# Kernel tuning notes

Hardware: AMD Instinct MI355X
Metric: run time of the kernel (lower is better)

Reference implementation:

```python
import jax, jax.numpy as jnp
import numpy as np

N_NODES = 50000


def setup_inputs() -> dict:
    key = jax.random.key(0)
    k1, k2, k3, k4, k5 = jax.random.split(key, 5)
    N, E, D_IN, D_OUT = N_NODES, 800000, 128, 128
    features = jax.random.normal(k1, (N, D_IN), dtype=jnp.float32)
    src = jax.random.randint(k2, (E,), 0, N, dtype=jnp.int32)
    dst = jax.random.randint(k3, (E,), 0, N, dtype=jnp.int32)
    # Kaiming-ish init for linear weights
    W_self = jax.random.normal(k4, (D_IN, D_OUT), dtype=jnp.float32) / np.sqrt(D_IN)
    W_neigh = jax.random.normal(k5, (D_IN, D_OUT), dtype=jnp.float32) / np.sqrt(D_IN)
    b = jnp.zeros((D_OUT,), dtype=jnp.float32)
    return {"features": features, "src": src, "dst": dst,
            "W_self": W_self, "W_neigh": W_neigh, "b": b}


def reference(features, src, dst, W_self, W_neigh, b):
    # DGL SAGEConv with 'mean' aggregator:
    #   h_neigh[v] = mean_{(u->v) in E} features[u]   (0 if in-degree 0)
    #   out = features @ W_self + h_neigh @ W_neigh + b
    N = features.shape[0]
    # gather source features along edges, then segment-sum into destinations
    neigh_sum = jax.ops.segment_sum(features[src], dst, num_segments=N)  # [N, D]
    deg = jax.ops.segment_sum(jnp.ones_like(dst, dtype=features.dtype), dst,
                              num_segments=N)  # [N]
    h_neigh = neigh_sum / jnp.maximum(deg, 1.0)[:, None]
    return features @ W_self + h_neigh @ W_neigh + b
```

## Files before the change

kernel.cpp:

```cpp
#include <hip/hip_runtime.h>

#define D 128
#define CAPN 64
#define HPAD 136

typedef __attribute__((ext_vector_type(8))) short bf16x8;
typedef __attribute__((ext_vector_type(4))) float f32x4;

__device__ __forceinline__ unsigned short f2bf(float f) {
    union { float f; unsigned int u; } c;
    c.f = f;
    unsigned int lsb = (c.u >> 16) & 1u;
    c.u += 0x7fffu + lsb;
    return (unsigned short)(c.u >> 16);
}

__device__ __forceinline__ float bf_lo(unsigned int x) {
    union { unsigned int u; float f; } c;
    c.u = x << 16;
    return c.f;
}
__device__ __forceinline__ float bf_hi(unsigned int x) {
    union { unsigned int u; float f; } c;
    c.u = x & 0xffff0000u;
    return c.f;
}

__global__ __launch_bounds__(256) void prep_kernel(const float* __restrict__ feat,
                                                   unsigned short* __restrict__ fb,
                                                   const float* __restrict__ Ws,
                                                   const float* __restrict__ Wn,
                                                   unsigned short* __restrict__ Wfrag,
                                                   int* __restrict__ deg,
                                                   int castB, int n8, int N) {
    int bid = blockIdx.x;
    int t   = threadIdx.x;
    if (bid < castB) {
        int i = bid * 256 + t;
        if (i >= n8) return;
        const float4* s = (const float4*)(feat + (size_t)i * 8);
        float4 a = s[0];
        float4 b = s[1];
        unsigned short pk[8];
        pk[0] = f2bf(a.x); pk[1] = f2bf(a.y); pk[2] = f2bf(a.z); pk[3] = f2bf(a.w);
        pk[4] = f2bf(b.x); pk[5] = f2bf(b.y); pk[6] = f2bf(b.z); pk[7] = f2bf(b.w);
        *(bf16x8*)(fb + (size_t)i * 8) = *(const bf16x8*)pk;
    } else if (bid < castB + 16) {
        int tid = (bid - castB) * 256 + t;
        int l  = tid & 63;
        int ks = (tid >> 6) & 7;
        int nt = tid >> 9;
        int n  = nt * 16 + (l & 15);
        int kb = ks * 32 + (l >> 4) * 8;
        unsigned short pk[8];
#pragma unroll
        for (int j = 0; j < 8; ++j) {
            int k = kb + j;
            float w = (k < 128) ? Ws[k * D + n] : Wn[(k - 128) * D + n];
            pk[j] = f2bf(w);
        }
        *(bf16x8*)(Wfrag + (size_t)tid * 8) = *(const bf16x8*)pk;
    } else {
        int i = (bid - castB - 16) * 256 + t;
        if (i < N) deg[i] = 0;
    }
}

__global__ __launch_bounds__(256) void edge_kernel(const int* __restrict__ src,
                                                   const int* __restrict__ dst,
                                                   int* __restrict__ deg,
                                                   unsigned short* __restrict__ bucket,
                                                   int E) {
    int e = blockIdx.x * 256 + threadIdx.x;
    if (e >= E) return;
    int d = dst[e];
    int s = src[e];
    int loc = atomicAdd(&deg[d], 1);
    if (loc < CAPN)
        bucket[(size_t)d * CAPN + loc] = (unsigned short)s;
}

__global__ __launch_bounds__(256) void gather_mfma_kernel(
        const unsigned short* __restrict__ fb,
        const unsigned short* __restrict__ bucket,
        const int* __restrict__ deg,
        const unsigned short* __restrict__ Wfrag,
        const float* __restrict__ bias,
        float* __restrict__ out, int N) {
    __shared__ unsigned short hL[16 * HPAD];

    int t    = threadIdx.x;
    int w    = t >> 6;
    int lane = t & 63;
    int g    = lane >> 4;
    int c    = lane & 15;
    int v0   = blockIdx.x * 16;
    int n0   = v0 + w * 4;

    int nd  = n0 + (lane & 3);
    int dn  = (nd < N) ? deg[nd] : 0;
    int idx_cur = (n0 < N) ? (int)bucket[(size_t)n0 * CAPN + lane] : 0;

    for (int nn = 0; nn < 4; ++nn) {
        int node  = n0 + nn;
        int dtrue = __shfl(dn, nn);
        int d     = (node < N) ? dtrue : 0;
        if (d > CAPN) d = CAPN;
        int idx_next = (nn < 3 && node + 1 < N)
                     ? (int)bucket[(size_t)(node + 1) * CAPN + lane] : 0;

        float acc[8];
#pragma unroll
        for (int j = 0; j < 8; ++j) acc[j] = 0.f;

        for (int i0 = 0; i0 < d; i0 += 16) {
            int i  = i0 + g;
            int u0 = __shfl(idx_cur, i & 63);
            int u1 = __shfl(idx_cur, (i + 4) & 63);
            int u2 = __shfl(idx_cur, (i + 8) & 63);
            int u3 = __shfl(idx_cur, (i + 12) & 63);
            bool b0 = (i < d), b1 = (i + 4 < d), b2 = (i + 8 < d), b3 = (i + 12 < d);
            uint4 x0, x1, x2, x3;
            if (b0) x0 = *(const uint4*)(fb + (size_t)u0 * D + c * 8);
            if (b1) x1 = *(const uint4*)(fb + (size_t)u1 * D + c * 8);
            if (b2) x2 = *(const uint4*)(fb + (size_t)u2 * D + c * 8);
            if (b3) x3 = *(const uint4*)(fb + (size_t)u3 * D + c * 8);
            if (b0) {
                acc[0] += bf_lo(x0.x); acc[1] += bf_hi(x0.x);
                acc[2] += bf_lo(x0.y); acc[3] += bf_hi(x0.y);
                acc[4] += bf_lo(x0.z); acc[5] += bf_hi(x0.z);
                acc[6] += bf_lo(x0.w); acc[7] += bf_hi(x0.w);
            }
            if (b1) {
                acc[0] += bf_lo(x1.x); acc[1] += bf_hi(x1.x);
                acc[2] += bf_lo(x1.y); acc[3] += bf_hi(x1.y);
                acc[4] += bf_lo(x1.z); acc[5] += bf_hi(x1.z);
                acc[6] += bf_lo(x1.w); acc[7] += bf_hi(x1.w);
            }
            if (b2) {
                acc[0] += bf_lo(x2.x); acc[1] += bf_hi(x2.x);
                acc[2] += bf_lo(x2.y); acc[3] += bf_hi(x2.y);
                acc[4] += bf_lo(x2.z); acc[5] += bf_hi(x2.z);
                acc[6] += bf_lo(x2.w); acc[7] += bf_hi(x2.w);
            }
            if (b3) {
                acc[0] += bf_lo(x3.x); acc[1] += bf_hi(x3.x);
                acc[2] += bf_lo(x3.y); acc[3] += bf_hi(x3.y);
                acc[4] += bf_lo(x3.z); acc[5] += bf_hi(x3.z);
                acc[6] += bf_lo(x3.w); acc[7] += bf_hi(x3.w);
            }
        }

#pragma unroll
        for (int j = 0; j < 8; ++j) {
            acc[j] += __shfl_xor(acc[j], 16);
            acc[j] += __shfl_xor(acc[j], 32);
        }

        if (g == 0) {
            float inv = (d > 0) ? 1.0f / (float)dtrue : 0.0f;
            unsigned short pk[8];
#pragma unroll
            for (int j = 0; j < 8; ++j) pk[j] = f2bf(acc[j] * inv);
            *(bf16x8*)&hL[(w * 4 + nn) * HPAD + c * 8] = *(const bf16x8*)pk;
        }
        idx_cur = idx_next;
    }
    __syncthreads();

    int lo16 = lane & 15;
    int quad = lane >> 4;
    int rowA = v0 + lo16;
    if (rowA > N - 1) rowA = N - 1;

    f32x4 accO[2];
#pragma unroll
    for (int ntl = 0; ntl < 2; ++ntl) accO[ntl] = (f32x4){0.f, 0.f, 0.f, 0.f};

#pragma unroll
    for (int ks = 0; ks < 8; ++ks) {
        bf16x8 a;
        if (ks < 4)
            a = *(const bf16x8*)(fb + (size_t)rowA * D + ks * 32 + quad * 8);
        else
            a = *(const bf16x8*)&hL[lo16 * HPAD + (ks - 4) * 32 + quad * 8];
        const unsigned short* wp = Wfrag + ((size_t)ks * 64 + lane) * 8;
#pragma unroll
        for (int ntl = 0; ntl < 2; ++ntl) {
            int nt = w * 2 + ntl;
            bf16x8 b = *(const bf16x8*)(wp + (size_t)nt * 4096);
            accO[ntl] = __builtin_amdgcn_mfma_f32_16x16x32_bf16(a, b, accO[ntl], 0, 0, 0);
        }
    }

#pragma unroll
    for (int ntl = 0; ntl < 2; ++ntl) {
        int n = (w * 2 + ntl) * 16 + lo16;
        float bvl = bias[n];
#pragma unroll
        for (int r = 0; r < 4; ++r) {
            int row = v0 + quad * 4 + r;
            if (row < N) out[(size_t)row * D + n] = accO[ntl][r] + bvl;
        }
    }
}

extern "C" void kernel_launch(void* const* d_in, const int* in_sizes, int n_in,
                              void* d_out, int out_size, void* d_ws, size_t ws_size,
                              hipStream_t stream) {
    const float* feat = (const float*)d_in[0];
    const int*   src  = (const int*)d_in[1];
    const int*   dst  = (const int*)d_in[2];
    const float* Ws   = (const float*)d_in[3];
    const float* Wn   = (const float*)d_in[4];
    const float* bias = (const float*)d_in[5];
    float*       out  = (float*)d_out;

    const int N = in_sizes[0] / D;
    const int E = in_sizes[1];
    const int castB = (N * D / 8 + 255) / 256;
    const int zeroB = (N + 255) / 256;

    int* deg = (int*)d_ws;
    unsigned short* bucket = (unsigned short*)(deg + N);
    size_t short_count = (size_t)N * CAPN;
    short_count = (short_count + 7) & ~(size_t)7;
    unsigned short* fb    = bucket + short_count;
    unsigned short* Wfrag = fb + (size_t)N * D;

    prep_kernel<<<castB + 16 + zeroB, 256, 0, stream>>>(feat, fb, Ws, Wn, Wfrag, deg,
                                                        castB, N * D / 8, N);
    edge_kernel<<<(E + 255) / 256, 256, 0, stream>>>(src, dst, deg, bucket, E);
    gather_mfma_kernel<<<(N + 15) / 16, 256, 0, stream>>>(fb, bucket, deg, Wfrag,
                                                          bias, out, N);
}
```

Baseline: 175.5 us.

## Restructure neighbor gather to full-row per wave with zero-row padding

The gather loop now has each lane load one 4-byte bf16 pair per neighbor, with the whole 64-lane wave covering a full 256-byte row. Neighbor indices come from readlane instead of shuffles, and sixteen loads are issued unconditionally per step. Out-of-range slots point at a new zeroed padding row at index N, so per-load predicates and the cross-group shuffle reduction go away. The self-feature A fragments are also preloaded before the gather to overlap their latency. The cost is more, smaller load instructions per edge and extra wasted loads when the degree is not a multiple of 16.

```diff
diff --git a/kernel.cpp b/kernel.cpp
--- a/kernel.cpp
+++ b/kernel.cpp
@@ -63,6 +63,8 @@
     } else {
         int i = (bid - castB - 16) * 256 + t;
         if (i < N) deg[i] = 0;
+        if (bid == castB + 16 && t < 64)
+            ((unsigned int*)(fb + (size_t)N * D))[t] = 0;
     }
 }
 
@@ -92,10 +94,17 @@
     int t    = threadIdx.x;
     int w    = t >> 6;
     int lane = t & 63;
-    int g    = lane >> 4;
-    int c    = lane & 15;
+    int lo16 = lane & 15;
+    int quad = lane >> 4;
     int v0   = blockIdx.x * 16;
     int n0   = v0 + w * 4;
+
+    int rowA = v0 + lo16;
+    if (rowA > N - 1) rowA = N - 1;
+    bf16x8 aself[4];
+#pragma unroll
+    for (int ks = 0; ks < 4; ++ks)
+        aself[ks] = *(const bf16x8*)(fb + (size_t)rowA * D + ks * 32 + quad * 8);
 
     int nd  = n0 + (lane & 3);
     int dn  = (nd < N) ? deg[nd] : 0;
@@ -109,69 +118,29 @@
         int idx_next = (nn < 3 && node + 1 < N)
                      ? (int)bucket[(size_t)(node + 1) * CAPN + lane] : 0;
 
-        float acc[8];
-#pragma unroll
-        for (int j = 0; j < 8; ++j) acc[j] = 0.f;
-
-        for (int i0 = 0; i0 < d; i0 += 16) {
-            int i  = i0 + g;
-            int u0 = __shfl(idx_cur, i & 63);
-            int u1 = __shfl(idx_cur, (i + 4) & 63);
-            int u2 = __shfl(idx_cur, (i + 8) & 63);
-            int u3 = __shfl(idx_cur, (i + 12) & 63);
-            bool b0 = (i < d), b1 = (i + 4 < d), b2 = (i + 8 < d), b3 = (i + 12 < d);
-            uint4 x0, x1, x2, x3;
-            if (b0) x0 = *(const uint4*)(fb + (size_t)u0 * D + c * 8);
-            if (b1) x1 = *(const uint4*)(fb + (size_t)u1 * D + c * 8);
-            if (b2) x2 = *(const uint4*)(fb + (size_t)u2 * D + c * 8);
-            if (b3) x3 = *(const uint4*)(fb + (size_t)u3 * D + c * 8);
-            if (b0) {
-                acc[0] += bf_lo(x0.x); acc[1] += bf_hi(x0.x);
-                acc[2] += bf_lo(x0.y); acc[3] += bf_hi(x0.y);
-                acc[4] += bf_lo(x0.z); acc[5] += bf_hi(x0.z);
-                acc[6] += bf_lo(x0.w); acc[7] += bf_hi(x0.w);
+        float a0 = 0.f, a1 = 0.f;
+        for (int e0 = 0; e0 < d; e0 += 16) {
+            unsigned int x[16];
+#pragma unroll
+            for (int j = 0; j < 16; ++j) {
+                int ue = __builtin_amdgcn_readlane(idx_cur, e0 + j);
+                ue = (e0 + j < d) ? ue : N;
+                x[j] = *(const unsigned int*)(fb + (size_t)ue * D + lane * 2);
             }
-            if (b1) {
-                acc[0] += bf_lo(x1.x); acc[1] += bf_hi(x1.x);
-                acc[2] += bf_lo(x1.y); acc[3] += bf_hi(x1.y);
-                acc[4] += bf_lo(x1.z); acc[5] += bf_hi(x1.z);
-                acc[6] += bf_lo(x1.w); acc[7] += bf_hi(x1.w);
+#pragma unroll
+            for (int j = 0; j < 16; ++j) {
+                a0 += bf_lo(x[j]);
+                a1 += bf_hi(x[j]);
             }
-            if (b2) {
-                acc[0] += bf_lo(x2.x); acc[1] += bf_hi(x2.x);
-                acc[2] += bf_lo(x2.y); acc[3] += bf_hi(x2.y);
-                acc[4] += bf_lo(x2.z); acc[5] += bf_hi(x2.z);
-                acc[6] += bf_lo(x2.w); acc[7] += bf_hi(x2.w);
-            }
-            if (b3) {
-                acc[0] += bf_lo(x3.x); acc[1] += bf_hi(x3.x);
-                acc[2] += bf_lo(x3.y); acc[3] += bf_hi(x3.y);
-                acc[4] += bf_lo(x3.z); acc[5] += bf_hi(x3.z);
-                acc[6] += bf_lo(x3.w); acc[7] += bf_hi(x3.w);
-            }
-        }
-
-#pragma unroll
-        for (int j = 0; j < 8; ++j) {
-            acc[j] += __shfl_xor(acc[j], 16);
-            acc[j] += __shfl_xor(acc[j], 32);
-        }
-
-        if (g == 0) {
-            float inv = (d > 0) ? 1.0f / (float)dtrue : 0.0f;
-            unsigned short pk[8];
-#pragma unroll
-            for (int j = 0; j < 8; ++j) pk[j] = f2bf(acc[j] * inv);
-            *(bf16x8*)&hL[(w * 4 + nn) * HPAD + c * 8] = *(const bf16x8*)pk;
-        }
+        }
+
+        float inv = (d > 0) ? 1.0f / (float)dtrue : 0.0f;
+        unsigned int pk = ((unsigned int)f2bf(a1 * inv) << 16)
+                        | (unsigned int)f2bf(a0 * inv);
+        *(unsigned int*)&hL[(w * 4 + nn) * HPAD + lane * 2] = pk;
         idx_cur = idx_next;
     }
     __syncthreads();
-
-    int lo16 = lane & 15;
-    int quad = lane >> 4;
-    int rowA = v0 + lo16;
-    if (rowA > N - 1) rowA = N - 1;
 
     f32x4 accO[2];
 #pragma unroll
@@ -181,7 +150,7 @@
     for (int ks = 0; ks < 8; ++ks) {
         bf16x8 a;
         if (ks < 4)
-            a = *(const bf16x8*)(fb + (size_t)rowA * D + ks * 32 + quad * 8);
+            a = aself[ks];
         else
             a = *(const bf16x8*)&hL[lo16 * HPAD + (ks - 4) * 32 + quad * 8];
         const unsigned short* wp = Wfrag + ((size_t)ks * 64 + lane) * 8;
@@ -226,7 +195,7 @@
     size_t short_count = (size_t)N * CAPN;
     short_count = (short_count + 7) & ~(size_t)7;
     unsigned short* fb    = bucket + short_count;
-    unsigned short* Wfrag = fb + (size_t)N * D;
+    unsigned short* Wfrag = fb + (size_t)(N + 1) * D;
 
     prep_kernel<<<castB + 16 + zeroB, 256, 0, stream>>>(feat, fb, Ws, Wn, Wfrag, deg,
                                                         castB, N * D / 8, N);
```

New measurement: 173.1 us. About the same (-1.4%).
